# Performance work log

Hardware: AMD Instinct MI355X
Metric: run time of the kernel (lower is better)

The kernel has to match this reference:

```python
import jax, jax.numpy as jnp
import numpy as np

N_QUBITS = 12
N_LAYERS = 3
BATCH = 512
N_ACTIONS = 2
TWO_PI = 2.0 * np.pi

# PennyLane default.qubit convention: wire 0 is the most significant bit.

def _dims(wire, n):
    return 2 ** wire, 2 ** (n - 1 - wire)

def _rx_batched(state, theta, wire, n):
    # theta: [B] per-sample angle (encoding layer)
    d0, d1 = _dims(wire, n)
    st = state.reshape(-1, d0, 2, d1)
    h = theta * 0.5
    c = jnp.cos(h)[:, None, None]
    s = jnp.sin(h)[:, None, None]
    s0, s1 = st[:, :, 0, :], st[:, :, 1, :]
    return jnp.stack([c * s0 - 1j * s * s1, -1j * s * s0 + c * s1], axis=2).reshape(state.shape)

def _ry(state, theta, wire, n):
    # theta: scalar shared weight
    d0, d1 = _dims(wire, n)
    st = state.reshape(-1, d0, 2, d1)
    h = theta * 0.5
    c, s = jnp.cos(h), jnp.sin(h)
    s0, s1 = st[:, :, 0, :], st[:, :, 1, :]
    return jnp.stack([c * s0 - s * s1, s * s0 + c * s1], axis=2).reshape(state.shape)

def _rz(state, theta, wire, n):
    d0, d1 = _dims(wire, n)
    st = state.reshape(-1, d0, 2, d1)
    h = theta * 0.5
    p0 = jnp.cos(h) - 1j * jnp.sin(h)
    p1 = jnp.cos(h) + 1j * jnp.sin(h)
    return jnp.stack([p0 * st[:, :, 0, :], p1 * st[:, :, 1, :]], axis=2).reshape(state.shape)

def _static_diags(n):
    # static (numpy) CZ-ring diagonal and PauliZ eigenvalue tables
    dim = 2 ** n
    idx = np.arange(dim)
    bits = (idx[None, :] >> (n - 1 - np.arange(n)[:, None])) & 1  # [n, dim]
    cz = np.ones(dim, np.float32)
    for w in range(n):
        cz *= 1.0 - 2.0 * (bits[w] & bits[(w + 1) % n]).astype(np.float32)
    z = (1.0 - 2.0 * bits).astype(np.float32)  # [n, dim]
    return jnp.asarray(cz, jnp.complex64), jnp.asarray(z)

def _forward(inputs, w_input2, w_output2, y_weights, z_weights):
    n = N_QUBITS
    B = inputs.shape[0]
    dim = 2 ** n
    cz_diag, z_eig = _static_diags(n)
    # input scaling + atan encoding angles, [B, n]
    ang = jnp.arctan(inputs * w_input2)
    # |0...0> batched state, [B, 2^n] complex64
    state = jnp.zeros((B, dim), jnp.complex64).at[:, 0].set(1.0)
    for l in range(N_LAYERS):
        # data_reupload=True -> encode every layer
        for w in range(n):
            state = _rx_batched(state, ang[:, w], w, n)
        for w in range(n):
            state = _ry(state, y_weights[l, w], w, n)
        for w in range(n):
            state = _rz(state, z_weights[l, w], w, n)
        state = state * cz_diag  # ring of CZ gates = diagonal +-1
    probs = state.real ** 2 + state.imag ** 2  # [B, 2^n]
    # n_output == 2: expvals of Z0Z1 and Z2Z3
    e0 = probs @ (z_eig[0] * z_eig[1])
    e1 = probs @ (z_eig[2] * z_eig[3])
    expvals = jnp.stack([e0, e1], axis=1)  # [B, 2]
    return (1.0 + expvals) * 0.5 * w_output2

def setup_inputs() -> dict:
    key = jax.random.key(0)
    k1, k2, k3, k4, k5 = jax.random.split(key, 5)
    return {
        'inputs': jax.random.normal(k1, (BATCH, N_QUBITS), jnp.float32),
        'w_input2': jax.random.normal(k2, (N_QUBITS,), jnp.float32),
        'w_output2': 90.0 + jax.random.normal(k3, (N_ACTIONS,), jnp.float32),
        'y_weights': jax.random.uniform(k4, (N_LAYERS, N_QUBITS), jnp.float32, 0.0, TWO_PI),
        'z_weights': jax.random.uniform(k5, (N_LAYERS, N_QUBITS), jnp.float32, 0.0, TWO_PI),
    }

def reference(inputs, w_input2, w_output2, y_weights, z_weights):
    return _forward(inputs, w_input2, w_output2, y_weights, z_weights)
```

## Files before the change

### kernel.cpp

```cpp
#include <hip/hip_runtime.h>
#include <math.h>

#define NQ 12
#define NB 512

typedef float2 cplx;
__device__ __forceinline__ cplx cmul(cplx a, cplx b) { return make_float2(a.x*b.x - a.y*b.y, a.x*b.y + a.y*b.x); }
__device__ __forceinline__ cplx cconj(cplx a) { return make_float2(a.x, -a.y); }
__device__ __forceinline__ cplx cadd(cplx a, cplx b) { return make_float2(a.x+b.x, a.y+b.y); }
__device__ __forceinline__ cplx csub(cplx a, cplx b) { return make_float2(a.x-b.x, a.y-b.y); }
__device__ __forceinline__ cplx cscale(cplx a, float s) { return make_float2(a.x*s, a.y*s); }
__device__ __forceinline__ cplx cneg(cplx a) { return make_float2(-a.x, -a.y); }

__global__ __launch_bounds__(64) void qdqn_kernel(
    const float* __restrict__ inputs,
    const float* __restrict__ w_input2,
    const float* __restrict__ w_output2,
    const float* __restrict__ y_weights,
    const float* __restrict__ z_weights,
    float* __restrict__ out)
{
    __shared__ float sP0[NQ], sP1[NQ], sDL[NQ], sZA[NQ], sA2[4];
    __shared__ cplx  sV0[NQ], sV1[NQ], sZB[NQ];
    __shared__ cplx  sA1[4], sB1[4], sEP[4], sB2[4];

    const int tid = threadIdx.x;
    const int blk = blockIdx.x;

    if (tid < NQ) {
        const int w = tid;
        float t  = inputs[blk * NQ + w] * w_input2[w];
        float hx = 0.5f * atanf(t);
        float cx, sx; __sincosf(hx, &sx, &cx);

        float hy0 = 0.5f * y_weights[w];
        float cy0, sy0; __sincosf(hy0, &sy0, &cy0);
        float hz0 = 0.5f * z_weights[w];
        float c0, s0; __sincosf(hz0, &s0, &c0);
        float ar = cy0 * cx, ai = sy0 * sx;
        cplx v0 = make_float2(c0 * ar + s0 * ai, c0 * ai - s0 * ar);
        float br = sy0 * cx, bi = -cy0 * sx;
        cplx v1 = make_float2(c0 * br - s0 * bi, c0 * bi + s0 * br);
        float p0 = v0.x * v0.x + v0.y * v0.y;
        float p1 = v1.x * v1.x + v1.y * v1.y;
        sV0[w] = v0; sV1[w] = v1; sP0[w] = p0; sP1[w] = p1; sDL[w] = p0 - p1;

        float hy1 = 0.5f * y_weights[NQ + w];
        float cy1, sy1; __sincosf(hy1, &sy1, &cy1);
        cplx A1 = make_float2(cy1 * cx, sy1 * sx);
        cplx B1 = make_float2(-sy1 * cx, -cy1 * sx);
        sZA[w] = (A1.x*A1.x + A1.y*A1.y) - (B1.x*B1.x + B1.y*B1.y);
        cplx bt = cmul(cconj(A1), B1);
        sZB[w] = make_float2(2.0f * bt.x, 2.0f * bt.y);

        if (w < 4) {
            sA1[w] = A1; sB1[w] = B1;
            float th = z_weights[NQ + w];
            float cth, sth; __sincosf(th, &sth, &cth);
            sEP[w] = make_float2(cth, sth);
            float hy2 = 0.5f * y_weights[2 * NQ + w];
            float cy2, sy2; __sincosf(hy2, &sy2, &cy2);
            cplx A2 = make_float2(cy2 * cx, sy2 * sx);
            cplx B2 = make_float2(-sy2 * cx, -cy2 * sx);
            sA2[w] = (A2.x*A2.x + A2.y*A2.y) - (B2.x*B2.x + B2.y*B2.y);
            cplx b2 = cmul(cconj(A2), B2);
            sB2[w] = make_float2(2.0f * b2.x, 2.0f * b2.y);
        }
    }
    __syncthreads();

    float eout = 0.0f;
    if (tid < 8) {
        const int obs = tid >> 2, term = tid & 3;
        const int p = obs * 2;
        const int wm1 = (p + 11) % 12, wp = p, wp1 = p + 1, wp2 = p + 2;
        const int wins[4] = { wm1, wp, wp1, wp2 };

        cplx dW[4][4];
        #pragma unroll
        for (int i = 0; i < 4; ++i) {
            dW[i][0] = make_float2(sP0[wins[i]], 0.0f);
            dW[i][1] = make_float2(0.0f, 0.0f);
            dW[i][2] = make_float2(0.0f, 0.0f);
            dW[i][3] = make_float2(sP1[wins[i]], 0.0f);
        }
        auto setKMN = [&](int i, int w, cplx k, cplx m, cplx n) {
            cplx v0 = sV0[w], v1 = sV1[w];
            dW[i][0] = cscale(k, sP0[w]);
            dW[i][1] = cmul(cmul(cconj(v0), m), v1);
            dW[i][2] = cmul(cmul(cconj(v1), n), v0);
            dW[i][3] = cscale(k, -sP1[w]);
        };
        auto setZ = [&](int i, int w) {
            cplx m = sZB[w];
            setKMN(i, w, make_float2(sZA[w], 0.0f), m, cconj(m));
        };
        auto setF = [&](int i, int w, int type) {
            cplx beta = cmul(sB2[w], sEP[w]);
            cplx gam = (type == 1) ? cneg(beta) : beta;
            cplx del = (type == 2) ? cneg(cconj(beta)) : cconj(beta);
            cplx A = sA1[w], B = sB1[w];
            cplx cA = cconj(A), cB = cconj(B);
            cplx k = cneg(cadd(cmul(gam, cmul(cA, cB)), cmul(del, cmul(A, B))));
            cplx m = csub(cmul(gam, cmul(cA, cA)), cmul(del, cmul(B, B)));
            cplx n = csub(cmul(del, cmul(A, A)), cmul(gam, cmul(cB, cB)));
            setKMN(i, w, k, m, n);
        };

        float coeff;
        if (term == 0)      { coeff = sA2[p] * sA2[p + 1]; setZ(1, wp);  setZ(2, wp1); }
        else if (term == 1) { coeff = sA2[p];              setF(2, wp1, 0); setZ(3, wp2); }
        else if (term == 2) { coeff = sA2[p + 1];          setZ(0, wm1); setF(1, wp, 0); }
        else                { coeff = 1.0f;                setZ(0, wm1); setF(1, wp, 1);
                                                           setF(2, wp1, 2); setZ(3, wp2); }

        const float dU = sDL[p + 3];
        const float dC = sDL[(p + 10) % 12];
        cplx t0 = make_float2(1.0f, 0.0f), t1 = make_float2(dU, 0.0f);
        cplx t2 = t1, t3 = t0;
        auto appD = [&](int i) {
            t0 = cmul(t0, dW[i][0]); t1 = cmul(t1, dW[i][1]);
            t2 = cmul(t2, dW[i][2]); t3 = cmul(t3, dW[i][3]);
        };
        auto bfly = [&]() {
            cplx a0 = cadd(t0, t1), a1 = csub(t0, t1);
            cplx a2 = cadd(t2, t3), a3 = csub(t2, t3);
            t0 = cadd(a0, a2); t1 = cadd(a1, a3);
            t2 = csub(a0, a2); t3 = csub(a1, a3);
        };
        appD(3); bfly(); appD(2); bfly(); appD(1); bfly(); appD(0);
        float E = t0.x + dC * (t1.x + t2.x) + t3.x;
        eout = coeff * E;
    }

    eout += __shfl_down(eout, 1);
    eout += __shfl_down(eout, 2);
    if (tid < 8 && (tid & 3) == 0) {
        const int obs = tid >> 2;
        out[blk * 2 + obs] = (1.0f + eout) * 0.5f * w_output2[obs];
    }
}

extern "C" void kernel_launch(void* const* d_in, const int* in_sizes, int n_in,
                              void* d_out, int out_size, void* d_ws, size_t ws_size,
                              hipStream_t stream) {
    const float* inputs    = (const float*)d_in[0];
    const float* w_input2  = (const float*)d_in[1];
    const float* w_output2 = (const float*)d_in[2];
    const float* y_weights = (const float*)d_in[3];
    const float* z_weights = (const float*)d_in[4];
    float* out = (float*)d_out;
    qdqn_kernel<<<NB, 64, 0, stream>>>(inputs, w_input2, w_output2,
                                       y_weights, z_weights, out);
}
```

Measured before the change: 9.686 us.

## Pack four batch samples per wavefront and replace shared memory with shuffles

Each 64-lane wavefront now handles four batch samples in 16-lane groups, so the launch shrinks from 512 blocks to 128. Per-wire values move between lanes with __shfl instead of going through shared memory behind __syncthreads. atan followed by sincos is replaced with an algebraic half-angle form built from rsqrtf. Every lane now computes all the layer-2 terms, which adds redundant ALU work and many shuffles.

```diff
diff --git a/kernel.cpp b/kernel.cpp
--- a/kernel.cpp
+++ b/kernel.cpp
@@ -1,8 +1,10 @@
 #include <hip/hip_runtime.h>
 #include <math.h>
 
-#define NQ 12
-#define NB 512
+#define NQ   12
+#define NB   512
+#define GPB  4
+#define NBLK (NB / GPB)
 
 typedef float2 cplx;
 __device__ __forceinline__ cplx cmul(cplx a, cplx b) { return make_float2(a.x*b.x - a.y*b.y, a.x*b.y + a.y*b.x); }
@@ -20,124 +22,137 @@
     const float* __restrict__ z_weights,
     float* __restrict__ out)
 {
-    __shared__ float sP0[NQ], sP1[NQ], sDL[NQ], sZA[NQ], sA2[4];
-    __shared__ cplx  sV0[NQ], sV1[NQ], sZB[NQ];
-    __shared__ cplx  sA1[4], sB1[4], sEP[4], sB2[4];
+    const int lane  = threadIdx.x & 63;
+    const int sub   = lane & 15;
+    const int base  = lane & 48;
+    const int batch = blockIdx.x * GPB + (lane >> 4);
 
-    const int tid = threadIdx.x;
-    const int blk = blockIdx.x;
+    const int w = (sub >= NQ) ? (sub - NQ) : sub;
 
-    if (tid < NQ) {
-        const int w = tid;
-        float t  = inputs[blk * NQ + w] * w_input2[w];
-        float hx = 0.5f * atanf(t);
-        float cx, sx; __sincosf(hx, &sx, &cx);
+    float t = inputs[batch * NQ + w] * w_input2[w];
+    float c  = rsqrtf(1.0f + t * t);
+    float rh = rsqrtf(0.5f * (1.0f + c));
+    float cx = 0.5f * (1.0f + c) * rh;
+    float sx = 0.5f * t * c * rh;
 
-        float hy0 = 0.5f * y_weights[w];
-        float cy0, sy0; __sincosf(hy0, &sy0, &cy0);
-        float hz0 = 0.5f * z_weights[w];
-        float c0, s0; __sincosf(hz0, &s0, &c0);
-        float ar = cy0 * cx, ai = sy0 * sx;
-        cplx v0 = make_float2(c0 * ar + s0 * ai, c0 * ai - s0 * ar);
-        float br = sy0 * cx, bi = -cy0 * sx;
-        cplx v1 = make_float2(c0 * br - s0 * bi, c0 * bi + s0 * br);
-        float p0 = v0.x * v0.x + v0.y * v0.y;
-        float p1 = v1.x * v1.x + v1.y * v1.y;
-        sV0[w] = v0; sV1[w] = v1; sP0[w] = p0; sP1[w] = p1; sDL[w] = p0 - p1;
+    float hy0 = 0.5f * y_weights[w];
+    float cy0, sy0; __sincosf(hy0, &sy0, &cy0);
+    float hz0 = 0.5f * z_weights[w];
+    float c0, s0; __sincosf(hz0, &s0, &c0);
+    float ar = cy0 * cx, ai = sy0 * sx;
+    cplx v0 = make_float2(c0 * ar + s0 * ai, c0 * ai - s0 * ar);
+    float br = sy0 * cx, bi = -cy0 * sx;
+    cplx v1 = make_float2(c0 * br - s0 * bi, c0 * bi + s0 * br);
+    float p0 = v0.x * v0.x + v0.y * v0.y;
+    float p1 = v1.x * v1.x + v1.y * v1.y;
+    float dl = p0 - p1;
 
-        float hy1 = 0.5f * y_weights[NQ + w];
-        float cy1, sy1; __sincosf(hy1, &sy1, &cy1);
-        cplx A1 = make_float2(cy1 * cx, sy1 * sx);
-        cplx B1 = make_float2(-sy1 * cx, -cy1 * sx);
-        sZA[w] = (A1.x*A1.x + A1.y*A1.y) - (B1.x*B1.x + B1.y*B1.y);
-        cplx bt = cmul(cconj(A1), B1);
-        sZB[w] = make_float2(2.0f * bt.x, 2.0f * bt.y);
+    float hy1 = 0.5f * y_weights[NQ + w];
+    float cy1, sy1; __sincosf(hy1, &sy1, &cy1);
+    cplx A1 = make_float2(cy1 * cx, sy1 * sx);
+    cplx B1 = make_float2(-sy1 * cx, -cy1 * sx);
+    float za = (A1.x*A1.x + A1.y*A1.y) - (B1.x*B1.x + B1.y*B1.y);
+    cplx bt = cmul(cconj(A1), B1);
+    cplx zb = make_float2(2.0f * bt.x, 2.0f * bt.y);
 
-        if (w < 4) {
-            sA1[w] = A1; sB1[w] = B1;
-            float th = z_weights[NQ + w];
-            float cth, sth; __sincosf(th, &sth, &cth);
-            sEP[w] = make_float2(cth, sth);
-            float hy2 = 0.5f * y_weights[2 * NQ + w];
-            float cy2, sy2; __sincosf(hy2, &sy2, &cy2);
-            cplx A2 = make_float2(cy2 * cx, sy2 * sx);
-            cplx B2 = make_float2(-sy2 * cx, -cy2 * sx);
-            sA2[w] = (A2.x*A2.x + A2.y*A2.y) - (B2.x*B2.x + B2.y*B2.y);
-            cplx b2 = cmul(cconj(A2), B2);
-            sB2[w] = make_float2(2.0f * b2.x, 2.0f * b2.y);
-        }
+    float th1 = z_weights[NQ + w];
+    float cth, sth; __sincosf(th1, &sth, &cth);
+    cplx ep = make_float2(cth, sth);
+    float hy2 = 0.5f * y_weights[2 * NQ + w];
+    float cy2, sy2; __sincosf(hy2, &sy2, &cy2);
+    cplx A2 = make_float2(cy2 * cx, sy2 * sx);
+    cplx B2 = make_float2(-sy2 * cx, -cy2 * sx);
+    float a2 = (A2.x*A2.x + A2.y*A2.y) - (B2.x*B2.x + B2.y*B2.y);
+    cplx b2c = cmul(cconj(A2), B2);
+    cplx b2 = make_float2(2.0f * b2c.x, 2.0f * b2c.y);
+
+    auto SHf = [&](const float& v, int ww) -> float { return __shfl(v, base + ww); };
+    auto SHc = [&](const cplx& v, int ww) -> cplx {
+        return make_float2(__shfl(v.x, base + ww), __shfl(v.y, base + ww));
+    };
+
+    const int obs = (sub >> 2) & 1, term = sub & 3;
+    const int p = obs * 2;
+    const int wm1 = (p + 11) % 12, wp = p, wp1 = p + 1, wp2 = p + 2;
+    const int wins[4] = { wm1, wp, wp1, wp2 };
+
+    float p0s[4], p1s[4], zas[4];
+    cplx  v0s[4], v1s[4], zbs[4];
+    #pragma unroll
+    for (int i = 0; i < 4; ++i) {
+        const int ww = wins[i];
+        p0s[i] = SHf(p0, ww);  p1s[i] = SHf(p1, ww);
+        v0s[i] = SHc(v0, ww);  v1s[i] = SHc(v1, ww);
+        zas[i] = SHf(za, ww);  zbs[i] = SHc(zb, ww);
     }
-    __syncthreads();
+    cplx A1w[2], B1w[2], betw[2];
+    #pragma unroll
+    for (int i = 0; i < 2; ++i) {
+        const int ww = p + i;
+        A1w[i] = SHc(A1, ww);  B1w[i] = SHc(B1, ww);
+        betw[i] = cmul(SHc(b2, ww), SHc(ep, ww));
+    }
+    const float a2p  = SHf(a2, p);
+    const float a2p1 = SHf(a2, p + 1);
+    const float dU   = SHf(dl, p + 3);
+    const float dC   = SHf(dl, (p == 0) ? 10 : 0);
 
-    float eout = 0.0f;
-    if (tid < 8) {
-        const int obs = tid >> 2, term = tid & 3;
-        const int p = obs * 2;
-        const int wm1 = (p + 11) % 12, wp = p, wp1 = p + 1, wp2 = p + 2;
-        const int wins[4] = { wm1, wp, wp1, wp2 };
+    cplx dW[4][4];
+    #pragma unroll
+    for (int i = 0; i < 4; ++i) {
+        dW[i][0] = make_float2(p0s[i], 0.0f);
+        dW[i][1] = make_float2(0.0f, 0.0f);
+        dW[i][2] = make_float2(0.0f, 0.0f);
+        dW[i][3] = make_float2(p1s[i], 0.0f);
+    }
+    auto setKMN = [&](int i, cplx k, cplx m, cplx n) {
+        dW[i][0] = cscale(k, p0s[i]);
+        dW[i][1] = cmul(cmul(cconj(v0s[i]), m), v1s[i]);
+        dW[i][2] = cmul(cmul(cconj(v1s[i]), n), v0s[i]);
+        dW[i][3] = cscale(k, -p1s[i]);
+    };
+    auto setZ = [&](int i) {
+        setKMN(i, make_float2(zas[i], 0.0f), zbs[i], cconj(zbs[i]));
+    };
+    auto setF = [&](int i, int fs, int type) {
+        cplx beta = betw[fs];
+        cplx gam = (type == 1) ? cneg(beta) : beta;
+        cplx del = (type == 2) ? cneg(cconj(beta)) : cconj(beta);
+        cplx A = A1w[fs], B = B1w[fs];
+        cplx cA = cconj(A), cB = cconj(B);
+        cplx k = cneg(cadd(cmul(gam, cmul(cA, cB)), cmul(del, cmul(A, B))));
+        cplx m = csub(cmul(gam, cmul(cA, cA)), cmul(del, cmul(B, B)));
+        cplx n = csub(cmul(del, cmul(A, A)), cmul(gam, cmul(cB, cB)));
+        setKMN(i, k, m, n);
+    };
 
-        cplx dW[4][4];
-        #pragma unroll
-        for (int i = 0; i < 4; ++i) {
-            dW[i][0] = make_float2(sP0[wins[i]], 0.0f);
-            dW[i][1] = make_float2(0.0f, 0.0f);
-            dW[i][2] = make_float2(0.0f, 0.0f);
-            dW[i][3] = make_float2(sP1[wins[i]], 0.0f);
-        }
-        auto setKMN = [&](int i, int w, cplx k, cplx m, cplx n) {
-            cplx v0 = sV0[w], v1 = sV1[w];
-            dW[i][0] = cscale(k, sP0[w]);
-            dW[i][1] = cmul(cmul(cconj(v0), m), v1);
-            dW[i][2] = cmul(cmul(cconj(v1), n), v0);
-            dW[i][3] = cscale(k, -sP1[w]);
-        };
-        auto setZ = [&](int i, int w) {
-            cplx m = sZB[w];
-            setKMN(i, w, make_float2(sZA[w], 0.0f), m, cconj(m));
-        };
-        auto setF = [&](int i, int w, int type) {
-            cplx beta = cmul(sB2[w], sEP[w]);
-            cplx gam = (type == 1) ? cneg(beta) : beta;
-            cplx del = (type == 2) ? cneg(cconj(beta)) : cconj(beta);
-            cplx A = sA1[w], B = sB1[w];
-            cplx cA = cconj(A), cB = cconj(B);
-            cplx k = cneg(cadd(cmul(gam, cmul(cA, cB)), cmul(del, cmul(A, B))));
-            cplx m = csub(cmul(gam, cmul(cA, cA)), cmul(del, cmul(B, B)));
-            cplx n = csub(cmul(del, cmul(A, A)), cmul(gam, cmul(cB, cB)));
-            setKMN(i, w, k, m, n);
-        };
+    float coeff;
+    if (term == 0)      { coeff = a2p * a2p1; setZ(1); setZ(2); }
+    else if (term == 1) { coeff = a2p;        setF(2, 1, 0); setZ(3); }
+    else if (term == 2) { coeff = a2p1;       setZ(0); setF(1, 0, 0); }
+    else                { coeff = 1.0f;       setZ(0); setF(1, 0, 1);
+                                              setF(2, 1, 2); setZ(3); }
 
-        float coeff;
-        if (term == 0)      { coeff = sA2[p] * sA2[p + 1]; setZ(1, wp);  setZ(2, wp1); }
-        else if (term == 1) { coeff = sA2[p];              setF(2, wp1, 0); setZ(3, wp2); }
-        else if (term == 2) { coeff = sA2[p + 1];          setZ(0, wm1); setF(1, wp, 0); }
-        else                { coeff = 1.0f;                setZ(0, wm1); setF(1, wp, 1);
-                                                           setF(2, wp1, 2); setZ(3, wp2); }
+    cplx t0 = make_float2(1.0f, 0.0f), t1 = make_float2(dU, 0.0f);
+    cplx t2 = t1, t3 = t0;
+    auto appD = [&](int i) {
+        t0 = cmul(t0, dW[i][0]); t1 = cmul(t1, dW[i][1]);
+        t2 = cmul(t2, dW[i][2]); t3 = cmul(t3, dW[i][3]);
+    };
+    auto bfly = [&]() {
+        cplx a0 = cadd(t0, t1), a1 = csub(t0, t1);
+        cplx a2v = cadd(t2, t3), a3 = csub(t2, t3);
+        t0 = cadd(a0, a2v); t1 = cadd(a1, a3);
+        t2 = csub(a0, a2v); t3 = csub(a1, a3);
+    };
+    appD(3); bfly(); appD(2); bfly(); appD(1); bfly(); appD(0);
+    float E = t0.x + dC * (t1.x + t2.x) + t3.x;
+    float eout = coeff * E;
 
-        const float dU = sDL[p + 3];
-        const float dC = sDL[(p + 10) % 12];
-        cplx t0 = make_float2(1.0f, 0.0f), t1 = make_float2(dU, 0.0f);
-        cplx t2 = t1, t3 = t0;
-        auto appD = [&](int i) {
-            t0 = cmul(t0, dW[i][0]); t1 = cmul(t1, dW[i][1]);
-            t2 = cmul(t2, dW[i][2]); t3 = cmul(t3, dW[i][3]);
-        };
-        auto bfly = [&]() {
-            cplx a0 = cadd(t0, t1), a1 = csub(t0, t1);
-            cplx a2 = cadd(t2, t3), a3 = csub(t2, t3);
-            t0 = cadd(a0, a2); t1 = cadd(a1, a3);
-            t2 = csub(a0, a2); t3 = csub(a1, a3);
-        };
-        appD(3); bfly(); appD(2); bfly(); appD(1); bfly(); appD(0);
-        float E = t0.x + dC * (t1.x + t2.x) + t3.x;
-        eout = coeff * E;
-    }
-
-    eout += __shfl_down(eout, 1);
-    eout += __shfl_down(eout, 2);
-    if (tid < 8 && (tid & 3) == 0) {
-        const int obs = tid >> 2;
-        out[blk * 2 + obs] = (1.0f + eout) * 0.5f * w_output2[obs];
+    eout += __shfl_xor(eout, 1);
+    eout += __shfl_xor(eout, 2);
+    if (sub < 8 && (sub & 3) == 0) {
+        out[batch * 2 + obs] = (1.0f + eout) * 0.5f * w_output2[obs];
     }
 }
 
@@ -150,6 +165,6 @@
     const float* y_weights = (const float*)d_in[3];
     const float* z_weights = (const float*)d_in[4];
     float* out = (float*)d_out;
-    qdqn_kernel<<<NB, 64, 0, stream>>>(inputs, w_input2, w_output2,
-                                       y_weights, z_weights, out);
+    qdqn_kernel<<<NBLK, 64, 0, stream>>>(inputs, w_input2, w_output2,
+                                         y_weights, z_weights, out);
 }
```

New measurement: 9.610 us. No clear change (-0.8%).
